# Kernel tuning notes

Hardware: AMD Instinct MI355X
Metric: run time of the kernel (lower is better)

## Reference

```python
import jax, jax.numpy as jnp
import numpy as np

EMBED_DIM = 1024
NUM_HEADS = 16
HEAD_DIM = EMBED_DIM // NUM_HEADS
SCALE = HEAD_DIM ** -0.5


def setup_inputs() -> dict:
    key = jax.random.key(0)
    k1, k2, k3 = jax.random.split(key, 3)
    B, S, E = 2, 2048, EMBED_DIM
    # xavier-uniform-like init scaled down for stability
    x = jax.random.normal(k1, (B, S, E), dtype=jnp.float32)
    w_qkv = jax.random.normal(k2, (3 * E, E), dtype=jnp.float32) * (E ** -0.5)
    w_out = jax.random.normal(k3, (E, E), dtype=jnp.float32) * (E ** -0.5)
    bias_qkv = jnp.zeros((3 * E,), dtype=jnp.float32)
    bias_out = jnp.zeros((E,), dtype=jnp.float32)
    return {"x": x, "w_qkv": w_qkv, "bias_qkv": bias_qkv, "w_out": w_out, "bias_out": bias_out}


def reference(x, w_qkv, bias_qkv, w_out, bias_out):
    B, S, E = x.shape
    H, D = NUM_HEADS, HEAD_DIM
    # fused QKV projection: nn.Linear semantics -> x @ w_qkv.T + bias
    qkv = jnp.einsum('bse,fe->bsf', x, w_qkv) + bias_qkv  # [B,S,3E]
    q, k, v = jnp.split(qkv, 3, axis=-1)
    # reshape to heads
    q = q.reshape(B, S, H, D)
    k = k.reshape(B, S, H, D)
    v = v.reshape(B, S, H, D)
    # scaled dot-product attention (non-causal)
    scores = jnp.einsum('bqhd,bkhd->bhqk', q, k) * SCALE  # [B,H,S,S]
    probs = jax.nn.softmax(scores, axis=-1)
    ctx = jnp.einsum('bhqk,bkhd->bqhd', probs, v).reshape(B, S, E)
    # output projection
    out = jnp.einsum('bse,fe->bsf', ctx, w_out) + bias_out
    return out
```

## Files before the change

kernel.cpp:

```cpp
#include <hip/hip_runtime.h>
#include <hip/hip_bf16.h>


typedef __bf16 bf16_t;
typedef __bf16 bf16x4 __attribute__((ext_vector_type(4)));
typedef __bf16 bf16x8 __attribute__((ext_vector_type(8)));
typedef float f32x4 __attribute__((ext_vector_type(4)));

#define MFMA16(a, b, c) __builtin_amdgcn_mfma_f32_16x16x32_bf16(a, b, c, 0, 0, 0)

static constexpr int Bn = 2;
static constexpr int S = 2048;
static constexpr int E = 1024;
static constexpr int H = 16;
static constexpr int Dh = 64;

__device__ __forceinline__ void gl_lds16(const bf16_t* g, bf16_t* l) {
  __builtin_amdgcn_global_load_lds(
      (const __attribute__((address_space(1))) unsigned int*)g,
      (__attribute__((address_space(3))) unsigned int*)l, 16, 0, 0);
}

__device__ __forceinline__ int detect_fp32(const unsigned short* p) {
  int cnt = 0;
#pragma unroll
  for (int j = 0; j < 32; j++) {
    const int e = (p[j] >> 7) & 0xFF;
    cnt += (e > 140) ? 1 : 0;
  }
  return cnt >= 2;
}

static constexpr int G0 = 4194304 / 8;
static constexpr int G1 = G0 + 3145728 / 8;
static constexpr int G2 = G1 + 3072 / 8;
static constexpr int G3 = G2 + 1048576 / 8;
static constexpr int G4 = G3 + 1024 / 8;

__global__ void convert_all(const void* __restrict__ s0, const void* __restrict__ s1,
                            const void* __restrict__ s2, const void* __restrict__ s3,
                            const void* __restrict__ s4, bf16_t* __restrict__ dst) {
  const int fp32 = detect_fp32((const unsigned short*)s0);
  const int stride = gridDim.x * blockDim.x;
  for (int i = blockIdx.x * blockDim.x + threadIdx.x; i < G4; i += stride) {
    const void* s;
    int off;
    if (i < G0)      { s = s0; off = i; }
    else if (i < G1) { s = s1; off = i - G0; }
    else if (i < G2) { s = s2; off = i - G1; }
    else if (i < G3) { s = s3; off = i - G2; }
    else             { s = s4; off = i - G3; }
    bf16x8 o;
    if (fp32) {
      const float* sp = (const float*)s + off * 8;
#pragma unroll
      for (int j = 0; j < 8; j++) o[j] = (bf16_t)sp[j];
    } else {
      o = *((const bf16x8*)s + off);
    }
    *(bf16x8*)(dst + (size_t)i * 8) = o;
  }
}

__global__ __launch_bounds__(256) void gemm_qkv(
    const bf16_t* __restrict__ X, const bf16_t* __restrict__ W,
    const bf16_t* __restrict__ bias,
    bf16_t* __restrict__ Qo, bf16_t* __restrict__ Ko, bf16_t* __restrict__ Vo) {
  __shared__ bf16_t Alds[16 * 512];
  __shared__ bf16_t Blds[16 * 512];
  const int tid = threadIdx.x;
  const int wave = tid >> 6, lane = tid & 63;
  const int lr = lane & 15, quad = lane >> 4;
  const int wm = wave >> 1, wn = wave & 1;
  const int m0 = blockIdx.y * 128, n0 = blockIdx.x * 128;
  constexpr int Kd = 1024;

  f32x4 acc[4][4] = {};
  for (int k0 = 0; k0 < Kd; k0 += 64) {
    __syncthreads();
#pragma unroll
    for (int i = 0; i < 4; i++) {
      const int fb = wave * 4 + i;
      const int mt = fb >> 1, kc = fb & 1;
      gl_lds16(X + (size_t)(m0 + mt * 16 + lr) * Kd + k0 + kc * 32 + quad * 8,
               &Alds[fb * 512]);
      gl_lds16(W + (size_t)(n0 + mt * 16 + lr) * Kd + k0 + kc * 32 + quad * 8,
               &Blds[fb * 512]);
    }
    __syncthreads();
#pragma unroll
    for (int kc = 0; kc < 2; kc++) {
      bf16x8 af[4], bfr[4];
#pragma unroll
      for (int mt = 0; mt < 4; mt++)
        af[mt] = *(const bf16x8*)&Alds[((wm * 4 + mt) * 2 + kc) * 512 + lane * 8];
#pragma unroll
      for (int nt = 0; nt < 4; nt++)
        bfr[nt] = *(const bf16x8*)&Blds[((wn * 4 + nt) * 2 + kc) * 512 + lane * 8];
#pragma unroll
      for (int mt = 0; mt < 4; mt++)
#pragma unroll
        for (int nt = 0; nt < 4; nt++)
          acc[mt][nt] = MFMA16(af[mt], bfr[nt], acc[mt][nt]);
    }
  }

  const int m0w = m0 + wm * 64, n0w = n0 + wn * 64;
#pragma unroll
  for (int nt = 0; nt < 4; nt++) {
    const int col = n0w + nt * 16 + lr;
    const float bs = (float)bias[col];
    const int which = col >> 10;
    const int e = col & 1023;
    const int h = e >> 6, d = e & 63;
#pragma unroll
    for (int mt = 0; mt < 4; mt++) {
      const int row0 = m0w + mt * 16 + quad * 4;
      const int b = row0 >> 11, s0 = row0 & 2047;
      if (which == 2) {
        bf16x4 v4;
#pragma unroll
        for (int r = 0; r < 4; r++) v4[r] = (bf16_t)(acc[mt][nt][r] + bs);
        *(bf16x4*)&Vo[((size_t)((b * H + h) * Dh + d)) * S + s0] = v4;
      } else {
        bf16_t* dst = (which == 0) ? Qo : Ko;
#pragma unroll
        for (int r = 0; r < 4; r++)
          dst[((size_t)((b * H + h) * S + (s0 + r))) * Dh + d] =
              (bf16_t)(acc[mt][nt][r] + bs);
      }
    }
  }
}

__global__ __launch_bounds__(256, 4) void attn_kernel(
    const bf16_t* __restrict__ Q, const bf16_t* __restrict__ K,
    const bf16_t* __restrict__ Vt, bf16_t* __restrict__ CTX) {
  __shared__ bf16_t Kl[2 * 8 * 512];
  __shared__ bf16_t Vl[2 * 8 * 512];
  __shared__ bf16_t Psh[4 * 16 * 64];

  const int tid = threadIdx.x;
  const int wave = tid >> 6, lane = tid & 63;
  const int lr = lane & 15, quad = lane >> 4;

  const int blk = blockIdx.x;
  const int bh = blk & 31;
  const int qt = blk >> 5;
  const int b = bh >> 4, h = bh & 15;

  const bf16_t* Qb = Q + (size_t)bh * S * Dh;
  const bf16_t* Kb = K + (size_t)bh * S * Dh;
  const bf16_t* Vb = Vt + (size_t)bh * Dh * S;

  const int q0 = qt * 64 + wave * 16;

  bf16x8 aq0 = *(const bf16x8*)(Qb + (size_t)(q0 + lr) * Dh + quad * 8);
  bf16x8 aq1 = *(const bf16x8*)(Qb + (size_t)(q0 + lr) * Dh + 32 + quad * 8);
#pragma unroll
  for (int j = 0; j < 8; j++) {
    aq0[j] = (bf16_t)((float)aq0[j] * 0.125f);
    aq1[j] = (bf16_t)((float)aq1[j] * 0.125f);
  }

  bf16x8 ones;
#pragma unroll
  for (int j = 0; j < 8; j++) ones[j] = (bf16_t)1.0f;

  bf16_t* pw = &Psh[wave * 16 * 64];
  const int xl = (lr & 7) << 3;

  const bf16_t* kg = Kb + (size_t)(wave * 16 + lr) * Dh + quad * 8;
  const bf16_t* vg = Vb + (size_t)(wave * 16 + lr) * S + quad * 8;

  f32x4 O[4] = {};
  f32x4 lacc = {};

  {
    gl_lds16(kg, &Kl[(wave * 2 + 0) * 512]);
    gl_lds16(kg + 32, &Kl[(wave * 2 + 1) * 512]);
    gl_lds16(vg, &Vl[(wave * 2 + 0) * 512]);
    gl_lds16(vg + 32, &Vl[(wave * 2 + 1) * 512]);
  }
  __syncthreads();

  int buf = 0;
#pragma unroll 2
  for (int sk0 = 0; sk0 < S; sk0 += 64) {
    const int bb = buf * 4096;
    const int nb = (buf ^ 1) * 4096;

    if (sk0 + 64 < S) {
      const int skn = sk0 + 64;
      gl_lds16(kg + (size_t)skn * Dh, &Kl[nb + (wave * 2 + 0) * 512]);
      gl_lds16(kg + (size_t)skn * Dh + 32, &Kl[nb + (wave * 2 + 1) * 512]);
      gl_lds16(vg + skn, &Vl[nb + (wave * 2 + 0) * 512]);
      gl_lds16(vg + skn + 32, &Vl[nb + (wave * 2 + 1) * 512]);
    }

    f32x4 sc[4];
#pragma unroll
    for (int nt = 0; nt < 4; nt++) {
      const bf16x8 k0f = *(const bf16x8*)&Kl[bb + (nt * 2 + 0) * 512 + lane * 8];
      const bf16x8 k1f = *(const bf16x8*)&Kl[bb + (nt * 2 + 1) * 512 + lane * 8];
      f32x4 z = {};
      z = MFMA16(aq0, k0f, z);
      sc[nt] = MFMA16(aq1, k1f, z);
    }

    bf16x8 vf[4][2];
#pragma unroll
    for (int dt = 0; dt < 4; dt++) {
      vf[dt][0] = *(const bf16x8*)&Vl[bb + (dt * 2 + 0) * 512 + lane * 8];
      vf[dt][1] = *(const bf16x8*)&Vl[bb + (dt * 2 + 1) * 512 + lane * 8];
    }

#pragma unroll
    for (int nt = 0; nt < 4; nt++)
#pragma unroll
      for (int r = 0; r < 4; r++) {
        const float p = __expf(sc[nt][r]);
        const int qr = quad * 4 + r;
        pw[qr * 64 + ((nt * 16 + lr) ^ ((qr & 7) << 3))] = (bf16_t)p;
      }

    const bf16x8 ap0 = *(const bf16x8*)&pw[lr * 64 + ((quad * 8) ^ xl)];
    const bf16x8 ap1 = *(const bf16x8*)&pw[lr * 64 + ((quad * 8 + 32) ^ xl)];
    lacc = MFMA16(ap0, ones, lacc);
    lacc = MFMA16(ap1, ones, lacc);
#pragma unroll
    for (int dt = 0; dt < 4; dt++) {
      O[dt] = MFMA16(ap0, vf[dt][0], O[dt]);
      O[dt] = MFMA16(ap1, vf[dt][1], O[dt]);
    }

    __syncthreads();
    buf ^= 1;
  }

  float rl[4];
#pragma unroll
  for (int r = 0; r < 4; r++) rl[r] = 1.0f / lacc[r];
#pragma unroll
  for (int dt = 0; dt < 4; dt++)
#pragma unroll
    for (int r = 0; r < 4; r++) {
      const int qrow = q0 + quad * 4 + r;
      CTX[(size_t)(b * S + qrow) * E + h * 64 + dt * 16 + lr] =
          (bf16_t)(O[dt][r] * rl[r]);
    }
}

__global__ __launch_bounds__(256) void gemm_out(
    const bf16_t* __restrict__ X, const bf16_t* __restrict__ W,
    const bf16_t* __restrict__ bias, void* __restrict__ Out,
    const void* __restrict__ xin) {
  __shared__ bf16_t Alds[8 * 512];
  __shared__ bf16_t Blds[16 * 512];
  const int tid = threadIdx.x;
  const int wave = tid >> 6, lane = tid & 63;
  const int lr = lane & 15, quad = lane >> 4;
  const int wm = wave >> 1, wn = wave & 1;
  const int m0 = blockIdx.y * 64, n0 = blockIdx.x * 128;
  constexpr int Kd = 1024;

  f32x4 acc[2][4] = {};
  for (int k0 = 0; k0 < Kd; k0 += 64) {
    __syncthreads();
#pragma unroll
    for (int kc = 0; kc < 2; kc++)
      gl_lds16(X + (size_t)(m0 + wave * 16 + lr) * Kd + k0 + kc * 32 + quad * 8,
               &Alds[(wave * 2 + kc) * 512]);
#pragma unroll
    for (int i = 0; i < 2; i++) {
      const int nt = wave * 2 + i;
#pragma unroll
      for (int kc = 0; kc < 2; kc++)
        gl_lds16(W + (size_t)(n0 + nt * 16 + lr) * Kd + k0 + kc * 32 + quad * 8,
                 &Blds[(nt * 2 + kc) * 512]);
    }
    __syncthreads();
#pragma unroll
    for (int kc = 0; kc < 2; kc++) {
      bf16x8 af[2], bfr[4];
#pragma unroll
      for (int mt = 0; mt < 2; mt++)
        af[mt] = *(const bf16x8*)&Alds[((wm * 2 + mt) * 2 + kc) * 512 + lane * 8];
#pragma unroll
      for (int nt = 0; nt < 4; nt++)
        bfr[nt] = *(const bf16x8*)&Blds[((wn * 4 + nt) * 2 + kc) * 512 + lane * 8];
#pragma unroll
      for (int mt = 0; mt < 2; mt++)
#pragma unroll
        for (int nt = 0; nt < 4; nt++)
          acc[mt][nt] = MFMA16(af[mt], bfr[nt], acc[mt][nt]);
    }
  }

  const int fp32 = detect_fp32((const unsigned short*)xin);
  const int m0w = m0 + wm * 32, n0w = n0 + wn * 64;
#pragma unroll
  for (int nt = 0; nt < 4; nt++) {
    const int col = n0w + nt * 16 + lr;
    const float bs = (float)bias[col];
#pragma unroll
    for (int mt = 0; mt < 2; mt++) {
#pragma unroll
      for (int r = 0; r < 4; r++) {
        const int row = m0w + mt * 16 + quad * 4 + r;
        const float v = acc[mt][nt][r] + bs;
        if (fp32)
          ((float*)Out)[(size_t)row * E + col] = v;
        else
          ((bf16_t*)Out)[(size_t)row * E + col] = (bf16_t)v;
      }
    }
  }
}

extern "C" void kernel_launch(void* const* d_in, const int* in_sizes, int n_in,
                              void* d_out, int out_size, void* d_ws, size_t ws_size,
                              hipStream_t stream) {
  const void* x = d_in[0];
  const void* w_qkv = d_in[1];
  const void* b_qkv = d_in[2];
  const void* w_out = d_in[3];
  const void* b_out = d_in[4];

  bf16_t* base = (bf16_t*)d_ws;
  const int N_X = Bn * S * E;
  const int N_WQ = 3 * E * E;
  const int N_BQ = 3 * E;
  const int N_WO = E * E;
  const int N_BO = E;
  bf16_t* xb = base;
  bf16_t* wqb = xb + N_X;
  bf16_t* bqb = wqb + N_WQ;
  bf16_t* wob = bqb + N_BQ;
  bf16_t* bob = wob + N_WO;
  const size_t QKV_ELEMS = (size_t)Bn * H * S * Dh;
  bf16_t* Qw = bob + N_BO;
  bf16_t* Kw = Qw + QKV_ELEMS;
  bf16_t* Vw = Kw + QKV_ELEMS;
  bf16_t* CTXw = Vw + QKV_ELEMS;

  convert_all<<<1024, 256, 0, stream>>>(x, w_qkv, b_qkv, w_out, b_out, xb);
  gemm_qkv<<<dim3(3 * E / 128, Bn * S / 128), 256, 0, stream>>>(xb, wqb, bqb, Qw, Kw, Vw);
  attn_kernel<<<32 * Bn * H, 256, 0, stream>>>(Qw, Kw, Vw, CTXw);
  gemm_out<<<dim3(E / 128, Bn * S / 64), 256, 0, stream>>>(CTXw, wob, bob, d_out, x);
}
```

Before: 229.4 us.

## Process 32 query rows per wave in attention to reuse K/V tiles

Each attention wave now handles two 16-row query tiles instead of one, so a workgroup covers 128 queries and the grid is halved. Every K and V fragment loaded from LDS feeds twice as many MFMAs, which halves global K/V traffic and LDS reads per query. In exchange, register pressure roughly doubles (the launch-bounds occupancy hint is lowered from 4 to 2) and only 512 workgroups remain to fill the GPU.

```diff
diff --git a/kernel.cpp b/kernel.cpp
--- a/kernel.cpp
+++ b/kernel.cpp
@@ -133,12 +133,12 @@
   }
 }
 
-__global__ __launch_bounds__(256, 4) void attn_kernel(
+__global__ __launch_bounds__(256, 2) void attn_kernel(
     const bf16_t* __restrict__ Q, const bf16_t* __restrict__ K,
     const bf16_t* __restrict__ Vt, bf16_t* __restrict__ CTX) {
   __shared__ bf16_t Kl[2 * 8 * 512];
   __shared__ bf16_t Vl[2 * 8 * 512];
-  __shared__ bf16_t Psh[4 * 16 * 64];
+  __shared__ bf16_t Psh[4 * 32 * 64];
 
   const int tid = threadIdx.x;
   const int wave = tid >> 6, lane = tid & 63;
@@ -153,28 +153,32 @@
   const bf16_t* Kb = K + (size_t)bh * S * Dh;
   const bf16_t* Vb = Vt + (size_t)bh * Dh * S;
 
-  const int q0 = qt * 64 + wave * 16;
-
-  bf16x8 aq0 = *(const bf16x8*)(Qb + (size_t)(q0 + lr) * Dh + quad * 8);
-  bf16x8 aq1 = *(const bf16x8*)(Qb + (size_t)(q0 + lr) * Dh + 32 + quad * 8);
-#pragma unroll
-  for (int j = 0; j < 8; j++) {
-    aq0[j] = (bf16_t)((float)aq0[j] * 0.125f);
-    aq1[j] = (bf16_t)((float)aq1[j] * 0.125f);
-  }
+  const int q0 = qt * 128 + wave * 32;
+
+  bf16x8 aq[2][2];
+#pragma unroll
+  for (int mt = 0; mt < 2; mt++)
+#pragma unroll
+    for (int kc = 0; kc < 2; kc++) {
+      bf16x8 t = *(const bf16x8*)(Qb + (size_t)(q0 + mt * 16 + lr) * Dh +
+                                  kc * 32 + quad * 8);
+#pragma unroll
+      for (int j = 0; j < 8; j++) t[j] = (bf16_t)((float)t[j] * 0.125f);
+      aq[mt][kc] = t;
+    }
 
   bf16x8 ones;
 #pragma unroll
   for (int j = 0; j < 8; j++) ones[j] = (bf16_t)1.0f;
 
-  bf16_t* pw = &Psh[wave * 16 * 64];
+  bf16_t* pw = &Psh[wave * 32 * 64];
   const int xl = (lr & 7) << 3;
 
   const bf16_t* kg = Kb + (size_t)(wave * 16 + lr) * Dh + quad * 8;
   const bf16_t* vg = Vb + (size_t)(wave * 16 + lr) * S + quad * 8;
 
-  f32x4 O[4] = {};
-  f32x4 lacc = {};
+  f32x4 O[2][4] = {};
+  f32x4 lacc[2] = {};
 
   {
     gl_lds16(kg, &Kl[(wave * 2 + 0) * 512]);
@@ -198,14 +202,17 @@
       gl_lds16(vg + skn + 32, &Vl[nb + (wave * 2 + 1) * 512]);
     }
 
-    f32x4 sc[4];
+    f32x4 sc[2][4];
 #pragma unroll
     for (int nt = 0; nt < 4; nt++) {
       const bf16x8 k0f = *(const bf16x8*)&Kl[bb + (nt * 2 + 0) * 512 + lane * 8];
       const bf16x8 k1f = *(const bf16x8*)&Kl[bb + (nt * 2 + 1) * 512 + lane * 8];
-      f32x4 z = {};
-      z = MFMA16(aq0, k0f, z);
-      sc[nt] = MFMA16(aq1, k1f, z);
+#pragma unroll
+      for (int mt = 0; mt < 2; mt++) {
+        f32x4 z = {};
+        z = MFMA16(aq[mt][0], k0f, z);
+        sc[mt][nt] = MFMA16(aq[mt][1], k1f, z);
+      }
     }
 
     bf16x8 vf[4][2];
@@ -216,39 +223,49 @@
     }
 
 #pragma unroll
-    for (int nt = 0; nt < 4; nt++)
+    for (int mt = 0; mt < 2; mt++)
+#pragma unroll
+      for (int nt = 0; nt < 4; nt++)
+#pragma unroll
+        for (int r = 0; r < 4; r++) {
+          const float p = __expf(sc[mt][nt][r]);
+          const int qr = mt * 16 + quad * 4 + r;
+          pw[qr * 64 + ((nt * 16 + lr) ^ ((qr & 7) << 3))] = (bf16_t)p;
+        }
+
+#pragma unroll
+    for (int mt = 0; mt < 2; mt++) {
+      const bf16x8 ap0 =
+          *(const bf16x8*)&pw[(mt * 16 + lr) * 64 + ((quad * 8) ^ xl)];
+      const bf16x8 ap1 =
+          *(const bf16x8*)&pw[(mt * 16 + lr) * 64 + ((quad * 8 + 32) ^ xl)];
+      lacc[mt] = MFMA16(ap0, ones, lacc[mt]);
+      lacc[mt] = MFMA16(ap1, ones, lacc[mt]);
+#pragma unroll
+      for (int dt = 0; dt < 4; dt++) {
+        O[mt][dt] = MFMA16(ap0, vf[dt][0], O[mt][dt]);
+        O[mt][dt] = MFMA16(ap1, vf[dt][1], O[mt][dt]);
+      }
+    }
+
+    __syncthreads();
+    buf ^= 1;
+  }
+
+#pragma unroll
+  for (int mt = 0; mt < 2; mt++) {
+    float rl[4];
+#pragma unroll
+    for (int r = 0; r < 4; r++) rl[r] = 1.0f / lacc[mt][r];
+#pragma unroll
+    for (int dt = 0; dt < 4; dt++)
 #pragma unroll
       for (int r = 0; r < 4; r++) {
-        const float p = __expf(sc[nt][r]);
-        const int qr = quad * 4 + r;
-        pw[qr * 64 + ((nt * 16 + lr) ^ ((qr & 7) << 3))] = (bf16_t)p;
-      }
-
-    const bf16x8 ap0 = *(const bf16x8*)&pw[lr * 64 + ((quad * 8) ^ xl)];
-    const bf16x8 ap1 = *(const bf16x8*)&pw[lr * 64 + ((quad * 8 + 32) ^ xl)];
-    lacc = MFMA16(ap0, ones, lacc);
-    lacc = MFMA16(ap1, ones, lacc);
-#pragma unroll
-    for (int dt = 0; dt < 4; dt++) {
-      O[dt] = MFMA16(ap0, vf[dt][0], O[dt]);
-      O[dt] = MFMA16(ap1, vf[dt][1], O[dt]);
-    }
-
-    __syncthreads();
-    buf ^= 1;
-  }
-
-  float rl[4];
-#pragma unroll
-  for (int r = 0; r < 4; r++) rl[r] = 1.0f / lacc[r];
-#pragma unroll
-  for (int dt = 0; dt < 4; dt++)
-#pragma unroll
-    for (int r = 0; r < 4; r++) {
-      const int qrow = q0 + quad * 4 + r;
-      CTX[(size_t)(b * S + qrow) * E + h * 64 + dt * 16 + lr] =
-          (bf16_t)(O[dt][r] * rl[r]);
-    }
+        const int qrow = q0 + mt * 16 + quad * 4 + r;
+        CTX[(size_t)(b * S + qrow) * E + h * 64 + dt * 16 + lr] =
+            (bf16_t)(O[mt][dt][r] * rl[r]);
+      }
+  }
 }
 
 __global__ __launch_bounds__(256) void gemm_out(
@@ -346,6 +363,6 @@
 
   convert_all<<<1024, 256, 0, stream>>>(x, w_qkv, b_qkv, w_out, b_out, xb);
   gemm_qkv<<<dim3(3 * E / 128, Bn * S / 128), 256, 0, stream>>>(xb, wqb, bqb, Qw, Kw, Vw);
-  attn_kernel<<<32 * Bn * H, 256, 0, stream>>>(Qw, Kw, Vw, CTXw);
+  attn_kernel<<<16 * Bn * H, 256, 0, stream>>>(Qw, Kw, Vw, CTXw);
   gemm_out<<<dim3(E / 128, Bn * S / 64), 256, 0, stream>>>(CTXw, wob, bob, d_out, x);
 }
```

After: 217.4 us. 5.2% less time.
